# Kernel tuning notes

Hardware: AMD Instinct MI355X
Metric: run time of the kernel (lower is better)

The kernel has to match this reference:

```python
import jax, jax.numpy as jnp
import numpy as np

NUM_PATCHES = 128  # K centers from farthest point sampling
PATCH_SIZE = 32    # neighbors per patch (KNN)


def setup_inputs() -> dict:
    key = jax.random.key(0)
    points = jax.random.normal(key, (32, 8192, 3), dtype=jnp.float32)
    return {"points": points}


def _fps(points, K):
    """Farthest point sampling. points: [B, N, 3] -> idx [B, K] (int32).
    Deterministic start at index 0 (original uses random_start_point=True;
    only the start index differs)."""
    B, N, _ = points.shape
    start = jnp.zeros((B,), dtype=jnp.int32)

    def step(carry, _):
        mind, last = carry  # mind: [B, N] running min sq-dist, last: [B]
        last_pt = jnp.take_along_axis(points, last[:, None, None], axis=1)[:, 0]  # [B, 3]
        d = jnp.sum((points - last_pt[:, None, :]) ** 2, axis=-1)  # [B, N]
        mind = jnp.minimum(mind, d)
        nxt = jnp.argmax(mind, axis=1).astype(jnp.int32)
        return (mind, nxt), last

    init = (jnp.full((B, N), jnp.inf, dtype=points.dtype), start)
    _, idxs = jax.lax.scan(step, init, None, length=K)  # [K, B]
    return jnp.transpose(idxs)  # [B, K]


def reference(points):
    # FPS center selection
    fps_idx = _fps(points, NUM_PATCHES)  # [B, K]
    centers = jnp.take_along_axis(points, fps_idx[:, :, None], axis=1)  # [B, K, 3]
    # Brute-force KNN: squared distances centers->points, [B, K, N]
    d2 = (jnp.sum(centers * centers, axis=-1)[:, :, None]
          + jnp.sum(points * points, axis=-1)[:, None, :]
          - 2.0 * jnp.einsum('bkd,bnd->bkn', centers, points))
    # k smallest distances, sorted ascending (top_k of negated d2 is descending)
    _, idx = jax.lax.top_k(-d2, PATCH_SIZE)  # [B, K, patch_size]
    return idx, centers
```

## Files before the change

### kernel.cpp

```cpp
#include <hip/hip_runtime.h>

#define BB 32
#define NN 8192
#define KK 128
#define PP 32
#define IDX_COUNT (BB * KK * PP)

#define DPP_RED_U64(v, CMP)                                                   \
    {                                                                         \
        _Pragma("unroll")                                                     \
        for (int s = 0; s < 6; ++s) {                                         \
            const int ctrl = (s == 0) ? 0x111 : (s == 1) ? 0x112 :            \
                             (s == 2) ? 0x114 : (s == 3) ? 0x118 :            \
                             (s == 4) ? 0x142 : 0x143;                        \
            unsigned lo = (unsigned)v, hi = (unsigned)(v >> 32);              \
            unsigned slo, shi;                                                \
            switch (ctrl) {                                                   \
            case 0x111:                                                       \
                slo = (unsigned)__builtin_amdgcn_update_dpp((int)lo, (int)lo, 0x111, 0xf, 0xf, false); \
                shi = (unsigned)__builtin_amdgcn_update_dpp((int)hi, (int)hi, 0x111, 0xf, 0xf, false); break; \
            case 0x112:                                                       \
                slo = (unsigned)__builtin_amdgcn_update_dpp((int)lo, (int)lo, 0x112, 0xf, 0xf, false); \
                shi = (unsigned)__builtin_amdgcn_update_dpp((int)hi, (int)hi, 0x112, 0xf, 0xf, false); break; \
            case 0x114:                                                       \
                slo = (unsigned)__builtin_amdgcn_update_dpp((int)lo, (int)lo, 0x114, 0xf, 0xf, false); \
                shi = (unsigned)__builtin_amdgcn_update_dpp((int)hi, (int)hi, 0x114, 0xf, 0xf, false); break; \
            case 0x118:                                                       \
                slo = (unsigned)__builtin_amdgcn_update_dpp((int)lo, (int)lo, 0x118, 0xf, 0xf, false); \
                shi = (unsigned)__builtin_amdgcn_update_dpp((int)hi, (int)hi, 0x118, 0xf, 0xf, false); break; \
            case 0x142:                                                       \
                slo = (unsigned)__builtin_amdgcn_update_dpp((int)lo, (int)lo, 0x142, 0xf, 0xf, false); \
                shi = (unsigned)__builtin_amdgcn_update_dpp((int)hi, (int)hi, 0x142, 0xf, 0xf, false); break; \
            default:                                                          \
                slo = (unsigned)__builtin_amdgcn_update_dpp((int)lo, (int)lo, 0x143, 0xf, 0xf, false); \
                shi = (unsigned)__builtin_amdgcn_update_dpp((int)hi, (int)hi, 0x143, 0xf, 0xf, false); break; \
            }                                                                 \
            const unsigned long long sv = ((unsigned long long)shi << 32) | slo; \
            if (sv CMP v) v = sv;                                             \
        }                                                                     \
    }

__device__ __forceinline__ unsigned long long readlane63_u64(unsigned long long v) {
    const unsigned lo = (unsigned)__builtin_amdgcn_readlane((int)(unsigned)v, 63);
    const unsigned hi = (unsigned)__builtin_amdgcn_readlane((int)(unsigned)(v >> 32), 63);
    return ((unsigned long long)hi << 32) | lo;
}

__global__ __launch_bounds__(512) void fps_kernel(
    const float* __restrict__ pts, float* __restrict__ out,
    float4* __restrict__ wsp)
{
#pragma clang fp contract(off)
    const int b = blockIdx.x;
    const int t = threadIdx.x;
    const float* p = pts + (size_t)b * NN * 3;

    __shared__ float pts3[NN * 3];
    __shared__ float cbuf[KK * 3];
    __shared__ unsigned long long wk[2][8];

    float px[16], py[16], pz[16], mind[16];
#pragma unroll
    for (int i = 0; i < 16; ++i) {
        const int idx = t + i * 512;
        const float x = p[idx * 3 + 0], y = p[idx * 3 + 1], z = p[idx * 3 + 2];
        px[i] = x; py[i] = y; pz[i] = z; mind[i] = __builtin_inff();
        pts3[idx * 3 + 0] = x; pts3[idx * 3 + 1] = y; pts3[idx * 3 + 2] = z;
        if (wsp) wsp[(size_t)b * NN + idx] =
            make_float4(x, y, z, (x * x + y * y) + z * z);
    }
    __syncthreads();

    float lx = pts3[0], ly = pts3[1], lz = pts3[2];
    if (t == 0) { cbuf[0] = lx; cbuf[1] = ly; cbuf[2] = lz; }
    const int lane = t & 63, wid = t >> 6;

    for (int k = 0; k < KK - 1; ++k) {
        float best = -1.0f; unsigned bidx = 0;
#pragma unroll
        for (int i = 0; i < 16; ++i) {
            const float dx = px[i] - lx, dy = py[i] - ly, dz = pz[i] - lz;
            const float d = (dx * dx + dy * dy) + dz * dz;
            const float m = mind[i] < d ? mind[i] : d;
            mind[i] = m;
            if (m > best) { best = m; bidx = (unsigned)(t + i * 512); }
        }
        union { float f; unsigned u; } cv; cv.f = best;
        unsigned long long key = ((unsigned long long)cv.u << 32)
                               | (0xFFFFFFFFu - bidx);
        DPP_RED_U64(key, >);
        if (lane == 63) wk[k & 1][wid] = key;
        __syncthreads();
        unsigned long long w = wk[k & 1][0];
#pragma unroll
        for (int i = 1; i < 8; ++i) {
            const unsigned long long o = wk[k & 1][i];
            if (o > w) w = o;
        }
        const unsigned last = 0xFFFFFFFFu - (unsigned)(w & 0xFFFFFFFFu);
        lx = pts3[last * 3 + 0];
        ly = pts3[last * 3 + 1];
        lz = pts3[last * 3 + 2];
        if (t == 0) {
            cbuf[(k + 1) * 3 + 0] = lx;
            cbuf[(k + 1) * 3 + 1] = ly;
            cbuf[(k + 1) * 3 + 2] = lz;
        }
    }
    __syncthreads();
    if (t < KK * 3)
        out[IDX_COUNT + b * (KK * 3) + t] = cbuf[t];
}

#define CACHE_INS(kk, m1, m2, m3, m4)                                   \
    {                                                                   \
        const bool c1 = (kk) < m1, c2 = (kk) < m2,                      \
                   c3 = (kk) < m3, c4 = (kk) < m4;                      \
        m4 = c3 ? m3 : (c4 ? (kk) : m4);                                \
        m3 = c2 ? m2 : (c3 ? (kk) : m3);                                \
        m2 = c1 ? m1 : (c2 ? (kk) : m2);                                \
        m1 = c1 ? (kk) : m1;                                            \
    }

template <bool USE_WS>
__global__ __launch_bounds__(1024) void knn_kernel(
    const float* __restrict__ pts, const float4* __restrict__ wsp_all,
    float* __restrict__ out)
{
#pragma clang fp contract(off)
    const int t = threadIdx.x, lane = t & 63, wid = t >> 6;
    const int blk = blockIdx.x;
    const int b = blk >> 3;
    const int bk = b * KK + (blk & 7) * 16 + wid;

    __shared__ float4 sp[NN];
    if (USE_WS) {
        const float4* wsp = wsp_all + (size_t)b * NN;
#pragma unroll
        for (int i = 0; i < 8; ++i) {
            const int idx = t + i * 1024;
            sp[idx] = wsp[idx];
        }
    } else {
        const float* p = pts + (size_t)b * NN * 3;
#pragma unroll
        for (int i = 0; i < 8; ++i) {
            const int idx = t + i * 1024;
            const float x = p[idx * 3 + 0], y = p[idx * 3 + 1], z = p[idx * 3 + 2];
            sp[idx] = make_float4(x, y, z, (x * x + y * y) + z * z);
        }
    }

    const float cx = out[IDX_COUNT + bk * 3 + 0];
    const float cy = out[IDX_COUNT + bk * 3 + 1];
    const float cz = out[IDX_COUNT + bk * 3 + 2];
    const float cc = (cx * cx + cy * cy) + cz * cz;
    __syncthreads();

    unsigned long long m1 = ~0ull, m2 = ~0ull, m3 = ~0ull, m4 = ~0ull;
#pragma unroll 4
    for (int i = 0; i < 128; ++i) {
        const int idx = lane + i * 64;
        const float4 q = sp[idx];
        const float dot = (cx * q.x + cy * q.y) + cz * q.z;
        float d2 = (cc + q.w) - (2.0f * dot);
        d2 = d2 + 0.0f;
        union { float f; unsigned u; } cv; cv.f = d2;
        unsigned u = cv.u;
        u = (u & 0x80000000u) ? ~u : (u | 0x80000000u);
        const unsigned long long kk =
            ((unsigned long long)u << 32) | (unsigned)idx;
        CACHE_INS(kk, m1, m2, m3, m4);
    }

    float resv = 0.0f;
    for (int j = 0; j < PP; ++j) {
        unsigned long long r = m1;
        DPP_RED_U64(r, <);
        const unsigned long long best = readlane63_u64(r);
        if (lane == j) resv = (float)(unsigned)(best & 0xFFFFFFFFu);
        if (m1 == best) { m1 = m2; m2 = m3; m3 = m4; m4 = ~0ull; }
        if (m1 == ~0ull) {
            for (int i = 0; i < 128; ++i) {
                const int idx = lane + i * 64;
                const float4 q = sp[idx];
                const float dot = (cx * q.x + cy * q.y) + cz * q.z;
                float d2 = (cc + q.w) - (2.0f * dot);
                d2 = d2 + 0.0f;
                union { float f; unsigned u; } cv; cv.f = d2;
                unsigned u = cv.u;
                u = (u & 0x80000000u) ? ~u : (u | 0x80000000u);
                const unsigned long long kk =
                    ((unsigned long long)u << 32) | (unsigned)idx;
                if (kk > best) CACHE_INS(kk, m1, m2, m3, m4);
            }
        }
    }
    if (lane < PP) out[(size_t)bk * PP + lane] = resv;
}

extern "C" void kernel_launch(void* const* d_in, const int* in_sizes, int n_in,
                              void* d_out, int out_size, void* d_ws, size_t ws_size,
                              hipStream_t stream) {
    const float* pts = (const float*)d_in[0];
    float* out = (float*)d_out;
    const bool use_ws = ws_size >= (size_t)BB * NN * sizeof(float4);
    float4* wsp = use_ws ? (float4*)d_ws : nullptr;

    fps_kernel<<<BB, 512, 0, stream>>>(pts, out, wsp);
    if (use_ws)
        knn_kernel<true><<<BB * 8, 1024, 0, stream>>>(pts, wsp, out);
    else
        knn_kernel<false><<<BB * 8, 1024, 0, stream>>>(pts, nullptr, out);
}
```

Before: 266.1 us.

## Fuse FPS and KNN into one kernel with flag-polled center streaming

Merges the FPS and KNN kernels into a single launch. FPS blocks publish each newly selected center to a workspace through agent-scope atomic stores, and KNN blocks spin-poll those words (initialised to 0xFFFFFFFF by a memset) so they can start the neighbor search while FPS is still running. This is meant to hide the serial FPS latency and remove the kernel boundary, but it depends on all FPS blocks being co-resident, since polling blocks could otherwise deadlock. It also uses 128KB of LDS per block, which limits occupancy.

```diff
diff --git a/kernel.cpp b/kernel.cpp
--- a/kernel.cpp
+++ b/kernel.cpp
@@ -5,6 +5,7 @@
 #define KK 128
 #define PP 32
 #define IDX_COUNT (BB * KK * PP)
+#define XCHG_BYTES (BB * KK * 3 * 4)
 
 #define DPP_RED_U64(v, CMP)                                                   \
     {                                                                         \
@@ -46,9 +47,173 @@
     return ((unsigned long long)hi << 32) | lo;
 }
 
+__device__ __forceinline__ void publish_word(unsigned* p, float v) {
+    __hip_atomic_store(p, __float_as_uint(v), __ATOMIC_RELAXED,
+                       __HIP_MEMORY_SCOPE_AGENT);
+}
+__device__ __forceinline__ float poll_word(const unsigned* p) {
+    unsigned u = __hip_atomic_load(p, __ATOMIC_RELAXED, __HIP_MEMORY_SCOPE_AGENT);
+    while (u == 0xFFFFFFFFu) {
+        __builtin_amdgcn_s_sleep(8);
+        u = __hip_atomic_load(p, __ATOMIC_RELAXED, __HIP_MEMORY_SCOPE_AGENT);
+    }
+    return __uint_as_float(u);
+}
+
+#define CACHE_INS(kk, m1, m2, m3, m4)                                   \
+    {                                                                   \
+        const bool c1 = (kk) < m1, c2 = (kk) < m2,                      \
+                   c3 = (kk) < m3, c4 = (kk) < m4;                      \
+        m4 = c3 ? m3 : (c4 ? (kk) : m4);                                \
+        m3 = c2 ? m2 : (c3 ? (kk) : m3);                                \
+        m2 = c1 ? m1 : (c2 ? (kk) : m2);                                \
+        m1 = c1 ? (kk) : m1;                                            \
+    }
+
+__global__ __launch_bounds__(512) void fused_kernel(
+    const float* __restrict__ pts, float* __restrict__ out,
+    unsigned* __restrict__ xchg)
+{
+#pragma clang fp contract(off)
+    __shared__ __align__(16) unsigned char smem_raw[131072];
+    const int t = threadIdx.x;
+    const int lane = t & 63, wid = t >> 6;
+
+    if (blockIdx.x < BB) {
+        const int b = blockIdx.x;
+        const float* p = pts + (size_t)b * NN * 3;
+        float* pts3 = (float*)smem_raw;
+        float* cbuf = (float*)(smem_raw + 98304);
+        unsigned long long* wkf =
+            (unsigned long long*)(smem_raw + 98304 + 1536);
+
+        if (t == 0) {
+            unsigned* dst = xchg + (unsigned)b * KK * 3u;
+            publish_word(dst + 0, p[0]);
+            publish_word(dst + 1, p[1]);
+            publish_word(dst + 2, p[2]);
+        }
+
+        float px[16], py[16], pz[16], mind[16];
+#pragma unroll
+        for (int i = 0; i < 16; ++i) {
+            const int idx = t + i * 512;
+            const float x = p[idx * 3 + 0], y = p[idx * 3 + 1], z = p[idx * 3 + 2];
+            px[i] = x; py[i] = y; pz[i] = z; mind[i] = __builtin_inff();
+            pts3[idx * 3 + 0] = x; pts3[idx * 3 + 1] = y; pts3[idx * 3 + 2] = z;
+        }
+        __syncthreads();
+
+        float lx = pts3[0], ly = pts3[1], lz = pts3[2];
+        if (t == 0) { cbuf[0] = lx; cbuf[1] = ly; cbuf[2] = lz; }
+
+        for (int k = 0; k < KK - 1; ++k) {
+            float best = -1.0f; unsigned bidx = 0;
+#pragma unroll
+            for (int i = 0; i < 16; ++i) {
+                const float dx = px[i] - lx, dy = py[i] - ly, dz = pz[i] - lz;
+                const float d = (dx * dx + dy * dy) + dz * dz;
+                const float m = mind[i] < d ? mind[i] : d;
+                mind[i] = m;
+                if (m > best) { best = m; bidx = (unsigned)(t + i * 512); }
+            }
+            union { float f; unsigned u; } cv; cv.f = best;
+            unsigned long long key = ((unsigned long long)cv.u << 32)
+                                   | (0xFFFFFFFFu - bidx);
+            DPP_RED_U64(key, >);
+            if (lane == 63) wkf[(k & 1) * 8 + wid] = key;
+            __syncthreads();
+            unsigned long long w = wkf[(k & 1) * 8];
+#pragma unroll
+            for (int i = 1; i < 8; ++i) {
+                const unsigned long long o = wkf[(k & 1) * 8 + i];
+                if (o > w) w = o;
+            }
+            const unsigned last = 0xFFFFFFFFu - (unsigned)(w & 0xFFFFFFFFu);
+            lx = pts3[last * 3 + 0];
+            ly = pts3[last * 3 + 1];
+            lz = pts3[last * 3 + 2];
+            if (t == 0) {
+                cbuf[(k + 1) * 3 + 0] = lx;
+                cbuf[(k + 1) * 3 + 1] = ly;
+                cbuf[(k + 1) * 3 + 2] = lz;
+                unsigned* dst = xchg + ((unsigned)b * KK + (unsigned)(k + 1)) * 3u;
+                publish_word(dst + 0, lx);
+                publish_word(dst + 1, ly);
+                publish_word(dst + 2, lz);
+            }
+        }
+        __syncthreads();
+        if (t < KK * 3)
+            out[IDX_COUNT + b * (KK * 3) + t] = cbuf[t];
+    } else {
+        const int blk = blockIdx.x - BB;
+        const int b = blk >> 2, kblk = blk & 3;
+        float4* sp = (float4*)smem_raw;
+        const float* p = pts + (size_t)b * NN * 3;
+#pragma unroll
+        for (int i = 0; i < 16; ++i) {
+            const int idx = t + i * 512;
+            const float x = p[idx * 3 + 0], y = p[idx * 3 + 1], z = p[idx * 3 + 2];
+            sp[idx] = make_float4(x, y, z, (x * x + y * y) + z * z);
+        }
+        __syncthreads();
+
+        for (int u = 0; u < 4; ++u) {
+            const int c = kblk + 4 * wid + 32 * u;
+            const unsigned* src = xchg + ((unsigned)b * KK + (unsigned)c) * 3u;
+            const float cx = poll_word(src + 0);
+            const float cy = poll_word(src + 1);
+            const float cz = poll_word(src + 2);
+            const float cc = (cx * cx + cy * cy) + cz * cz;
+
+            unsigned long long m1 = ~0ull, m2 = ~0ull, m3 = ~0ull, m4 = ~0ull;
+#pragma unroll 4
+            for (int i = 0; i < 128; ++i) {
+                const int idx = lane + i * 64;
+                const float4 q = sp[idx];
+                const float dot = (cx * q.x + cy * q.y) + cz * q.z;
+                float d2 = (cc + q.w) - (2.0f * dot);
+                d2 = d2 + 0.0f;
+                union { float f; unsigned u; } cv; cv.f = d2;
+                unsigned uu = cv.u;
+                uu = (uu & 0x80000000u) ? ~uu : (uu | 0x80000000u);
+                const unsigned long long kk2 =
+                    ((unsigned long long)uu << 32) | (unsigned)idx;
+                CACHE_INS(kk2, m1, m2, m3, m4);
+            }
+
+            float resv = 0.0f;
+            for (int j = 0; j < PP; ++j) {
+                unsigned long long r = m1;
+                DPP_RED_U64(r, <);
+                const unsigned long long best = readlane63_u64(r);
+                if (lane == j) resv = (float)(unsigned)(best & 0xFFFFFFFFu);
+                if (m1 == best) { m1 = m2; m2 = m3; m3 = m4; m4 = ~0ull; }
+                if (m1 == ~0ull) {
+                    for (int i = 0; i < 128; ++i) {
+                        const int idx = lane + i * 64;
+                        const float4 q = sp[idx];
+                        const float dot = (cx * q.x + cy * q.y) + cz * q.z;
+                        float d2 = (cc + q.w) - (2.0f * dot);
+                        d2 = d2 + 0.0f;
+                        union { float f; unsigned u; } cv; cv.f = d2;
+                        unsigned uu = cv.u;
+                        uu = (uu & 0x80000000u) ? ~uu : (uu | 0x80000000u);
+                        const unsigned long long kk2 =
+                            ((unsigned long long)uu << 32) | (unsigned)idx;
+                        if (kk2 > best) CACHE_INS(kk2, m1, m2, m3, m4);
+                    }
+                }
+            }
+            if (lane < PP)
+                out[(size_t)(b * KK + c) * PP + lane] = resv;
+        }
+    }
+}
+
 __global__ __launch_bounds__(512) void fps_kernel(
-    const float* __restrict__ pts, float* __restrict__ out,
-    float4* __restrict__ wsp)
+    const float* __restrict__ pts, float* __restrict__ out)
 {
 #pragma clang fp contract(off)
     const int b = blockIdx.x;
@@ -66,8 +231,6 @@
         const float x = p[idx * 3 + 0], y = p[idx * 3 + 1], z = p[idx * 3 + 2];
         px[i] = x; py[i] = y; pz[i] = z; mind[i] = __builtin_inff();
         pts3[idx * 3 + 0] = x; pts3[idx * 3 + 1] = y; pts3[idx * 3 + 2] = z;
-        if (wsp) wsp[(size_t)b * NN + idx] =
-            make_float4(x, y, z, (x * x + y * y) + z * z);
     }
     __syncthreads();
 
@@ -112,20 +275,8 @@
         out[IDX_COUNT + b * (KK * 3) + t] = cbuf[t];
 }
 
-#define CACHE_INS(kk, m1, m2, m3, m4)                                   \
-    {                                                                   \
-        const bool c1 = (kk) < m1, c2 = (kk) < m2,                      \
-                   c3 = (kk) < m3, c4 = (kk) < m4;                      \
-        m4 = c3 ? m3 : (c4 ? (kk) : m4);                                \
-        m3 = c2 ? m2 : (c3 ? (kk) : m3);                                \
-        m2 = c1 ? m1 : (c2 ? (kk) : m2);                                \
-        m1 = c1 ? (kk) : m1;                                            \
-    }
-
-template <bool USE_WS>
 __global__ __launch_bounds__(1024) void knn_kernel(
-    const float* __restrict__ pts, const float4* __restrict__ wsp_all,
-    float* __restrict__ out)
+    const float* __restrict__ pts, float* __restrict__ out)
 {
 #pragma clang fp contract(off)
     const int t = threadIdx.x, lane = t & 63, wid = t >> 6;
@@ -134,21 +285,12 @@
     const int bk = b * KK + (blk & 7) * 16 + wid;
 
     __shared__ float4 sp[NN];
-    if (USE_WS) {
-        const float4* wsp = wsp_all + (size_t)b * NN;
-#pragma unroll
-        for (int i = 0; i < 8; ++i) {
-            const int idx = t + i * 1024;
-            sp[idx] = wsp[idx];
-        }
-    } else {
-        const float* p = pts + (size_t)b * NN * 3;
-#pragma unroll
-        for (int i = 0; i < 8; ++i) {
-            const int idx = t + i * 1024;
-            const float x = p[idx * 3 + 0], y = p[idx * 3 + 1], z = p[idx * 3 + 2];
-            sp[idx] = make_float4(x, y, z, (x * x + y * y) + z * z);
-        }
+    const float* p = pts + (size_t)b * NN * 3;
+#pragma unroll
+    for (int i = 0; i < 8; ++i) {
+        const int idx = t + i * 1024;
+        const float x = p[idx * 3 + 0], y = p[idx * 3 + 1], z = p[idx * 3 + 2];
+        sp[idx] = make_float4(x, y, z, (x * x + y * y) + z * z);
     }
 
     const float cx = out[IDX_COUNT + bk * 3 + 0];
@@ -204,12 +346,12 @@
                               hipStream_t stream) {
     const float* pts = (const float*)d_in[0];
     float* out = (float*)d_out;
-    const bool use_ws = ws_size >= (size_t)BB * NN * sizeof(float4);
-    float4* wsp = use_ws ? (float4*)d_ws : nullptr;
-
-    fps_kernel<<<BB, 512, 0, stream>>>(pts, out, wsp);
-    if (use_ws)
-        knn_kernel<true><<<BB * 8, 1024, 0, stream>>>(pts, wsp, out);
-    else
-        knn_kernel<false><<<BB * 8, 1024, 0, stream>>>(pts, nullptr, out);
-}
+
+    if (ws_size >= (size_t)XCHG_BYTES) {
+        hipMemsetAsync(d_ws, 0xFF, XCHG_BYTES, stream);
+        fused_kernel<<<BB + BB * 4, 512, 0, stream>>>(pts, out, (unsigned*)d_ws);
+    } else {
+        fps_kernel<<<BB, 512, 0, stream>>>(pts, out);
+        knn_kernel<<<BB * 8, 1024, 0, stream>>>(pts, out);
+    }
+}
```

New measurement: 235.7 us. -11.4%, faster.
